# Kernel tuning notes

Hardware: AMD Instinct MI355X
Metric: run time of the kernel (lower is better)

Reference implementation:

```python
import jax, jax.numpy as jnp
import numpy as np

N, T_PLUS_1, D_IN, WV, HID, V = 64, 33, 1024, 512, 1024, 32000
NULL_IDX = 0


def setup_inputs() -> dict:
    key = jax.random.key(0)
    ks = jax.random.split(key, 9)
    return {
        "features": jax.random.normal(ks[0], (N, D_IN, 4, 4), jnp.float32),
        "captions": jax.random.randint(ks[1], (N, T_PLUS_1), 0, V),
        "W_embed": jax.random.normal(ks[2], (V, WV), jnp.float32) / np.float32(np.sqrt(V)),
        "Wx": jax.random.normal(ks[3], (WV, 4 * HID), jnp.float32) / np.float32(np.sqrt(WV)),
        "Wh": jax.random.normal(ks[4], (HID, 4 * HID), jnp.float32) / np.float32(np.sqrt(HID)),
        "Wattn": jax.random.normal(ks[5], (HID, 4 * HID), jnp.float32) / np.float32(np.sqrt(HID)),
        "b": jnp.zeros((4 * HID,), jnp.float32),
        "W_proj": jax.random.normal(ks[6], (D_IN, HID), jnp.float32) / np.float32(np.sqrt(D_IN)),
        "b_proj": jnp.zeros((HID,), jnp.float32),
        "W_out": jax.random.normal(ks[7], (HID, V), jnp.float32) / np.float32(np.sqrt(HID)),
        "b_out": jnp.zeros((V,), jnp.float32),
    }


def reference(features, captions, W_embed, Wx, Wh, Wattn, b, W_proj, b_proj, W_out, b_out):
    n, _ = captions.shape
    cap_in = captions[:, :-1]   # [N, T]
    cap_out = captions[:, 1:]   # [N, T]

    # project_input applied channel-last: A is [N, H, 4, 4]
    A = jnp.einsum('ndhw,dk->nkhw', features, W_proj) + b_proj[None, :, None, None]
    h0 = A.mean(axis=(2, 3))  # [N, H]
    c0 = h0
    hdim = h0.shape[1]
    A_flat = A.reshape(n, hdim, -1)  # [N, H, P] with P = 16 grid cells
    inv_sqrt_h = jnp.float32(1.0 / np.sqrt(hdim))

    x = W_embed[cap_in]  # [N, T, WV]

    def step(carry, x_t):
        prev_h, prev_c = carry
        # dot-product attention over the spatial grid
        s = jnp.einsum('nh,nhp->np', prev_h, A_flat) * inv_sqrt_h
        w = jax.nn.softmax(s, axis=-1)
        attn = jnp.einsum('nhp,np->nh', A_flat, w)
        # LSTM gating
        a = x_t @ Wx + prev_h @ Wh + attn @ Wattn + b
        i = jax.nn.sigmoid(a[:, :hdim])
        f = jax.nn.sigmoid(a[:, hdim:2 * hdim])
        o = jax.nn.sigmoid(a[:, 2 * hdim:3 * hdim])
        g = jnp.tanh(a[:, 3 * hdim:])
        next_c = f * prev_c + i * g
        next_h = o * jnp.tanh(next_c)
        return (next_h, next_c), next_h

    _, hs = jax.lax.scan(step, (h0, c0), x.transpose(1, 0, 2))  # hs: [T, N, H]
    h = hs.transpose(1, 0, 2)  # [N, T, H]

    scores = h @ W_out + b_out  # [N, T, V]
    logp = jax.nn.log_softmax(scores, axis=-1)
    nll = -jnp.take_along_axis(logp, cap_out[..., None], axis=-1)[..., 0]  # [N, T]
    mask = (cap_out != NULL_IDX).astype(nll.dtype)
    loss = jnp.sum(nll * mask) / n
    return loss
```

## Files before the change

### kernel.cpp

```cpp
#include <hip/hip_runtime.h>
#include <hip/hip_bf16.h>
#include <math.h>

typedef __attribute__((ext_vector_type(8))) short short8;
typedef __attribute__((ext_vector_type(4))) float f32x4;
typedef unsigned short ushort_t;
typedef unsigned int uint_t;

typedef __attribute__((address_space(1))) const void gvoid_t;
typedef __attribute__((address_space(3))) void lvoid_t;

#define VTILES 125

static __device__ __forceinline__ ushort_t f2b(float f){
  __hip_bfloat16 h = __float2bfloat16(f);
  return *reinterpret_cast<ushort_t*>(&h);
}
static __device__ __forceinline__ float b2f(ushort_t u){
  __hip_bfloat16 h = *reinterpret_cast<__hip_bfloat16*>(&u);
  return __bfloat162float(h);
}
static __device__ __forceinline__ float sigmoidf_(float x){ return 1.0f/(1.0f+__expf(-x)); }

__global__ void k_transpose_cvt(const float* __restrict__ src, ushort_t* __restrict__ dst,
                                int C, int dstride, int dcoloff) {
  __shared__ ushort_t tile[64][72];
  int cb = blockIdx.x * 64, rb = blockIdx.y * 64;
  int tid = threadIdx.x;
  for (int it = 0; it < 4; ++it) {
    int e = tid + it*256;
    int row = e >> 4;
    int seg = e & 15;
    float4 v = *reinterpret_cast<const float4*>(&src[(size_t)(rb+row)*C + cb + seg*4]);
    tile[seg*4+0][row] = f2b(v.x);
    tile[seg*4+1][row] = f2b(v.y);
    tile[seg*4+2][row] = f2b(v.z);
    tile[seg*4+3][row] = f2b(v.w);
  }
  __syncthreads();
  for (int it = 0; it < 2; ++it) {
    int e = tid + it*256;
    int cl = e >> 3;
    int seg = e & 7;
    uint4 v = *reinterpret_cast<uint4*>(&tile[cl][seg*8]);
    *reinterpret_cast<uint4*>(&dst[(size_t)(cb+cl)*dstride + dcoloff + rb + seg*8]) = v;
  }
}

__global__ void k_featT(const float* __restrict__ feat, ushort_t* __restrict__ fBT) {
  __shared__ ushort_t t[16][264];
  int n = blockIdx.x;
  int tid = threadIdx.x;
  for (int it = 0; it < 4; ++it) {
    int d = it*256 + tid;
    const float* src = &feat[((size_t)n*1024 + d)*16];
    #pragma unroll
    for (int q = 0; q < 4; ++q) {
      float4 v = *reinterpret_cast<const float4*>(&src[q*4]);
      t[q*4+0][tid] = f2b(v.x);
      t[q*4+1][tid] = f2b(v.y);
      t[q*4+2][tid] = f2b(v.z);
      t[q*4+3][tid] = f2b(v.w);
    }
    __syncthreads();
    #pragma unroll
    for (int w = 0; w < 2; ++w) {
      int e = tid + w*256;
      int p = e >> 5;
      int seg = e & 31;
      uint4 v = *reinterpret_cast<uint4*>(&t[p][seg*8]);
      *reinterpret_cast<uint4*>(&fBT[((size_t)n*16 + p)*1024 + it*256 + seg*8]) = v;
    }
    __syncthreads();
  }
}

__global__ void k_embed(const int* __restrict__ captions, const float* __restrict__ W_embed,
                        ushort_t* __restrict__ xb) {
  int e = (blockIdx.x*256 + threadIdx.x) * 4;
  int nt = e >> 9;
  int n = nt >> 5, t = nt & 31;
  int col = e & 511;
  int tok = captions[n*33 + t];
  float4 v = *reinterpret_cast<const float4*>(&W_embed[(size_t)tok*512 + col]);
  ushort4 o; o.x=f2b(v.x); o.y=f2b(v.y); o.z=f2b(v.z); o.w=f2b(v.w);
  *reinterpret_cast<ushort4*>(&xb[e]) = o;
}

__global__ void k_projmm(const ushort_t* __restrict__ WprojT, const ushort_t* __restrict__ fBT,
                         const float* __restrict__ b_proj, float* __restrict__ A_flat,
                         ushort_t* __restrict__ Abt, float* __restrict__ hbuf) {
  __shared__ ushort_t As[64*64];
  __shared__ ushort_t Bs[64*64];
  int kt = blockIdx.x, nt = blockIdx.y;
  int k0 = kt*64, n0 = nt*64;
  int tid = threadIdx.x;
  int wave = tid>>6, lane = tid&63, lr = lane&15, lg = lane>>4;
  int srow = lane>>3, sxor8 = ((lane&7)^srow)*8;
  f32x4 acc[4];
  #pragma unroll
  for (int nf=0;nf<4;++nf) acc[nf] = (f32x4){0.f,0.f,0.f,0.f};
  for (int kc = 0; kc < 1024; kc += 64){
    __syncthreads();
    #pragma unroll
    for (int u = 0; u < 2; ++u){
      int r0 = wave*16 + u*8;
      const ushort_t* srcA = &WprojT[(size_t)(k0 + r0 + srow)*1024 + kc + sxor8];
      const ushort_t* srcB = &fBT[(size_t)(n0 + r0 + srow)*1024 + kc + sxor8];
      __builtin_amdgcn_global_load_lds((gvoid_t*)srcA, (lvoid_t*)&As[r0*64], 16, 0, 0);
      __builtin_amdgcn_global_load_lds((gvoid_t*)srcB, (lvoid_t*)&Bs[r0*64], 16, 0, 0);
    }
    __syncthreads();
    #pragma unroll
    for (int kk = 0; kk < 2; ++kk){
      int swz = (((kk*4 + lg) ^ (lr & 7)) * 8);
      short8 af = *reinterpret_cast<short8*>(&As[(wave*16 + lr)*64 + swz]);
      #pragma unroll
      for (int nf = 0; nf < 4; ++nf){
        short8 bf = *reinterpret_cast<short8*>(&Bs[(nf*16 + lr)*64 + swz]);
        acc[nf] = __builtin_amdgcn_mfma_f32_16x16x32_bf16(af, bf, acc[nf], 0, 0, 0);
      }
    }
  }
  #pragma unroll
  for (int nf=0;nf<4;++nf){
    int ncol = n0 + nf*16 + lr;
    int nidx = ncol >> 4, p = ncol & 15;
    ushort4 ab;
    #pragma unroll
    for (int r=0;r<4;++r){
      int kh = k0 + wave*16 + lg*4 + r;
      float val = acc[nf][r] + b_proj[kh];
      A_flat[((size_t)nidx*1024 + kh)*16 + p] = val;
      (&ab.x)[r] = f2b(val);
      float s = val;
      s += __shfl_xor(s, 1, 64);
      s += __shfl_xor(s, 2, 64);
      s += __shfl_xor(s, 4, 64);
      s += __shfl_xor(s, 8, 64);
      if (lr == 0) hbuf[(nt*4 + nf)*1024 + kh] = s * (1.f/16.f);
    }
    *reinterpret_cast<ushort4*>(&Abt[(size_t)ncol*1024 + k0 + wave*16 + lg*4]) = ab;
  }
}

__global__ void k_pmm(const ushort_t* __restrict__ WcatT, const ushort_t* __restrict__ Abt,
                      ushort_t* __restrict__ P3) {
  __shared__ ushort_t As[64*64];
  __shared__ ushort_t Bs[64*64];
  __shared__ ushort_t Dt2[64][72];
  int jt = blockIdx.x, nt = blockIdx.y;
  int j0 = jt*64, n0 = nt*64;
  int tid = threadIdx.x;
  int wave = tid>>6, lane = tid&63, lr = lane&15, lg = lane>>4;
  int srow = lane>>3, sxor8 = ((lane&7)^srow)*8;
  f32x4 acc[4];
  #pragma unroll
  for (int nf=0;nf<4;++nf) acc[nf] = (f32x4){0.f,0.f,0.f,0.f};
  for (int kc = 0; kc < 1024; kc += 64){
    __syncthreads();
    #pragma unroll
    for (int u = 0; u < 2; ++u){
      int r0 = wave*16 + u*8;
      const ushort_t* srcA = &WcatT[(size_t)(j0 + r0 + srow)*2560 + 1536 + kc + sxor8];
      const ushort_t* srcB = &Abt[(size_t)(n0 + r0 + srow)*1024 + kc + sxor8];
      __builtin_amdgcn_global_load_lds((gvoid_t*)srcA, (lvoid_t*)&As[r0*64], 16, 0, 0);
      __builtin_amdgcn_global_load_lds((gvoid_t*)srcB, (lvoid_t*)&Bs[r0*64], 16, 0, 0);
    }
    __syncthreads();
    #pragma unroll
    for (int kk = 0; kk < 2; ++kk){
      int swz = (((kk*4 + lg) ^ (lr & 7)) * 8);
      short8 af = *reinterpret_cast<short8*>(&As[(wave*16 + lr)*64 + swz]);
      #pragma unroll
      for (int nf = 0; nf < 4; ++nf){
        short8 bf = *reinterpret_cast<short8*>(&Bs[(nf*16 + lr)*64 + swz]);
        acc[nf] = __builtin_amdgcn_mfma_f32_16x16x32_bf16(af, bf, acc[nf], 0, 0, 0);
      }
    }
  }
  __syncthreads();
  #pragma unroll
  for (int nf=0;nf<4;++nf)
    #pragma unroll
    for (int r=0;r<4;++r)
      Dt2[wave*16 + lg*4 + r][nf*16 + lr] = f2b(acc[nf][r]);
  __syncthreads();
  #pragma unroll
  for (int it=0; it<2; ++it){
    int e = it*256 + tid;
    int row = e >> 3, seg = e & 7;
    uint4 v = *reinterpret_cast<uint4*>(&Dt2[row][seg*8]);
    *reinterpret_cast<uint4*>(&P3[(((size_t)nt*4 + (seg>>1))*4096 + j0 + row)*16 + (seg&1)*8]) = v;
  }
}

__global__ void k_xmm(const ushort_t* __restrict__ WcatT, const ushort_t* __restrict__ xb,
                      ushort_t* __restrict__ xpre) {
  __shared__ ushort_t As[64*64];
  __shared__ ushort_t Bs[64*64];
  __shared__ float Dt[64][68];
  int jt = blockIdx.x, mt = blockIdx.y;
  int j0 = jt*64, m0 = mt*64;
  int tid = threadIdx.x;
  int wave = tid>>6, lane = tid&63, lr = lane&15, lg = lane>>4;
  int srow = lane>>3, sxor8 = ((lane&7)^srow)*8;
  f32x4 acc[4];
  #pragma unroll
  for (int nf=0;nf<4;++nf) acc[nf] = (f32x4){0.f,0.f,0.f,0.f};
  for (int kc = 0; kc < 512; kc += 64){
    __syncthreads();
    #pragma unroll
    for (int u = 0; u < 2; ++u){
      int r0 = wave*16 + u*8;
      const ushort_t* srcA = &WcatT[(size_t)(j0 + r0 + srow)*2560 + kc + sxor8];
      const ushort_t* srcB = &xb[(size_t)(m0 + r0 + srow)*512 + kc + sxor8];
      __builtin_amdgcn_global_load_lds((gvoid_t*)srcA, (lvoid_t*)&As[r0*64], 16, 0, 0);
      __builtin_amdgcn_global_load_lds((gvoid_t*)srcB, (lvoid_t*)&Bs[r0*64], 16, 0, 0);
    }
    __syncthreads();
    #pragma unroll
    for (int kk = 0; kk < 2; ++kk){
      int swz = (((kk*4 + lg) ^ (lr & 7)) * 8);
      short8 af = *reinterpret_cast<short8*>(&As[(wave*16 + lr)*64 + swz]);
      #pragma unroll
      for (int nf = 0; nf < 4; ++nf){
        short8 bf = *reinterpret_cast<short8*>(&Bs[(nf*16 + lr)*64 + swz]);
        acc[nf] = __builtin_amdgcn_mfma_f32_16x16x32_bf16(af, bf, acc[nf], 0, 0, 0);
      }
    }
  }
  __syncthreads();
  #pragma unroll
  for (int nf=0; nf<4; ++nf)
    #pragma unroll
    for (int r=0;r<4;++r)
      Dt[nf*16+lr][wave*16 + lg*4 + r] = acc[nf][r];
  __syncthreads();
  #pragma unroll
  for (int it=0; it<4; ++it){
    int e = tid + it*256;
    int nrow = e >> 4, seg = e & 15;
    float4 v = *reinterpret_cast<float4*>(&Dt[nrow][seg*4]);
    ushort4 o; o.x=f2b(v.x); o.y=f2b(v.y); o.z=f2b(v.z); o.w=f2b(v.w);
    *reinterpret_cast<ushort4*>(&xpre[(size_t)(m0+nrow)*4096 + j0 + seg*4]) = o;
  }
}

__global__ void k_gate(int i, const ushort_t* __restrict__ xpre, const float* __restrict__ a_part,
                       const float* __restrict__ bvec, const ushort_t* __restrict__ P3,
                       const float* __restrict__ A_flat, const float* __restrict__ hbuf,
                       float* __restrict__ cbuf, const float* __restrict__ sp_rd,
                       float* __restrict__ sp_wr, ushort_t* __restrict__ hbf,
                       ushort_t* __restrict__ hall) {
  __shared__ float wvLds[16];
  __shared__ float wred[4][16];
  int n = blockIdx.x >> 2, sp = blockIdx.x & 3;
  int tid = threadIdx.x;
  int wave = tid>>6, lane = tid&63;
  int k = sp*256 + tid;
  float hv;
  if (i == 0){
    hv = hbuf[n*1024 + k];
    cbuf[n*1024 + k] = hv;
    hbf[n*1024 + k] = f2b(hv);
  } else {
    if (tid < 16){
      float sv = (sp_rd[(n*4+0)*16+tid] + sp_rd[(n*4+1)*16+tid] +
                  sp_rd[(n*4+2)*16+tid] + sp_rd[(n*4+3)*16+tid]) * (1.f/32.f);
      float m = sv;
      #pragma unroll
      for (int d=1; d<16; d<<=1) m = fmaxf(m, __shfl_xor(m, d, 64));
      float e = __expf(sv - m);
      float s = e;
      #pragma unroll
      for (int d=1; d<16; d<<=1) s += __shfl_xor(s, d, 64);
      wvLds[tid] = e / s;
    }
    __syncthreads();
    float wv[16];
    #pragma unroll
    for (int p=0;p<16;++p) wv[p] = wvLds[p];
    float av[4];
    #pragma unroll
    for (int g=0;g<4;++g){
      int j = g*1024 + k;
      float x = bvec[j] + b2f(xpre[(size_t)(n*32 + (i-1))*4096 + j]);
      #pragma unroll
      for (int ks=0;ks<8;++ks) x += a_part[((size_t)ks*64 + n)*4096 + j];
      const ushort_t* pp = &P3[((size_t)n*4096 + j)*16];
      short8 p0 = *reinterpret_cast<const short8*>(pp);
      short8 p1 = *reinterpret_cast<const short8*>(pp+8);
      #pragma unroll
      for (int p=0;p<8;++p) x += wv[p]*b2f((ushort_t)p0[p]);
      #pragma unroll
      for (int p=0;p<8;++p) x += wv[8+p]*b2f((ushort_t)p1[p]);
      av[g]=x;
    }
    float ig=sigmoidf_(av[0]), fg=sigmoidf_(av[1]), og=sigmoidf_(av[2]), gg=tanhf(av[3]);
    float c = fg*cbuf[n*1024+k] + ig*gg;
    hv = og*tanhf(c);
    cbuf[n*1024+k] = c;
    hall[((size_t)n*32 + (i-1))*1024 + k] = f2b(hv);
    if (i < 32) hbf[n*1024+k] = f2b(hv);
  }
  if (i == 32) return;
  float sacc[16];
  const float* An = &A_flat[((size_t)n*1024 + k)*16];
  #pragma unroll
  for (int p=0;p<16;p+=4){
    float4 a4 = *reinterpret_cast<const float4*>(&An[p]);
    sacc[p] = hv*a4.x; sacc[p+1] = hv*a4.y; sacc[p+2] = hv*a4.z; sacc[p+3] = hv*a4.w;
  }
  #pragma unroll
  for (int d=1; d<64; d<<=1)
    #pragma unroll
    for (int p=0;p<16;++p) sacc[p] += __shfl_xor(sacc[p], d, 64);
  if (lane == 0)
    #pragma unroll
    for (int p=0;p<16;++p) wred[wave][p] = sacc[p];
  __syncthreads();
  if (tid < 16)
    sp_wr[(n*4+sp)*16 + tid] = wred[0][tid]+wred[1][tid]+wred[2][tid]+wred[3][tid];
}

__global__ void k_mm(const ushort_t* __restrict__ WcatT, const ushort_t* __restrict__ hbf,
                     float* __restrict__ a_part) {
  __shared__ ushort_t As[64*64];
  __shared__ ushort_t Bs[64*64];
  __shared__ float Dt[64][68];
  int jt = blockIdx.x, ks = blockIdx.y;
  int j0 = jt*64;
  int tid = threadIdx.x;
  int wave = tid>>6, lane = tid&63, lr = lane&15, lg = lane>>4;
  int srow = lane>>3, sxor8 = ((lane&7)^srow)*8;
  f32x4 acc[4];
  #pragma unroll
  for (int nf=0;nf<4;++nf) acc[nf] = (f32x4){0.f,0.f,0.f,0.f};
  for (int kc = 0; kc < 128; kc += 64){
    __syncthreads();
    #pragma unroll
    for (int u = 0; u < 2; ++u){
      int r0 = wave*16 + u*8;
      const ushort_t* srcA = &WcatT[(size_t)(j0 + r0 + srow)*2560 + 512 + ks*128 + kc + sxor8];
      const ushort_t* srcB = &hbf[(size_t)(r0 + srow)*1024 + ks*128 + kc + sxor8];
      __builtin_amdgcn_global_load_lds((gvoid_t*)srcA, (lvoid_t*)&As[r0*64], 16, 0, 0);
      __builtin_amdgcn_global_load_lds((gvoid_t*)srcB, (lvoid_t*)&Bs[r0*64], 16, 0, 0);
    }
    __syncthreads();
    #pragma unroll
    for (int kk = 0; kk < 2; ++kk){
      int swz = (((kk*4 + lg) ^ (lr & 7)) * 8);
      short8 af = *reinterpret_cast<short8*>(&As[(wave*16 + lr)*64 + swz]);
      #pragma unroll
      for (int nf = 0; nf < 4; ++nf){
        short8 bf = *reinterpret_cast<short8*>(&Bs[(nf*16 + lr)*64 + swz]);
        acc[nf] = __builtin_amdgcn_mfma_f32_16x16x32_bf16(af, bf, acc[nf], 0, 0, 0);
      }
    }
  }
  __syncthreads();
  #pragma unroll
  for (int nf=0; nf<4; ++nf)
    #pragma unroll
    for (int r=0;r<4;++r)
      Dt[nf*16+lr][wave*16 + lg*4 + r] = acc[nf][r];
  __syncthreads();
  #pragma unroll
  for (int it=0; it<4; ++it){
    int e = tid + it*256;
    int nrow = e >> 4, seg = e & 15;
    float4 v = *reinterpret_cast<float4*>(&Dt[nrow][seg*4]);
    *reinterpret_cast<float4*>(&a_part[((size_t)ks*64 + nrow)*4096 + j0 + seg*4]) = v;
  }
}

__global__ void __launch_bounds__(512, 2)
k_score(const ushort_t* __restrict__ WoutT, const ushort_t* __restrict__ hall,
        const float* __restrict__ b_out,
        float* __restrict__ pmax, float* __restrict__ psum) {
  __shared__ ushort_t A_lds[3][16384];
  __shared__ ushort_t B_lds[3][8192];
  __shared__ float bLds[256];
  __shared__ float pmLds[2][128];
  __shared__ float psLds[2][128];

  int bid = blockIdx.x;
  int wg = (bid & 7) * 250 + (bid >> 3);
  int vb = wg >> 4, rb = wg & 15;
  size_t v0 = (size_t)vb * 256, r0 = (size_t)rb * 128;
  int tid = threadIdx.x;
  int wid = tid >> 6, lane = tid & 63;
  int wr = wid >> 2, wc = wid & 3;
  int lr = lane & 15, lg = lane >> 4;
  int srow = lane >> 3, sxor8 = ((lane & 7) ^ srow) * 8;

  const ushort_t* Abase = WoutT + v0*1024 + (size_t)srow*1024 + sxor8;
  const ushort_t* Bbase = hall  + r0*1024 + (size_t)srow*1024 + sxor8;

  auto stA = [&](int set, int u, int t){
    __builtin_amdgcn_global_load_lds(
      (gvoid_t*)(Abase + (size_t)(u*64 + wid*8)*1024 + t*64),
      (lvoid_t*)&A_lds[set][(u*64 + wid*8)*64], 16, 0, 0);
  };
  auto stB = [&](int set, int u, int t){
    __builtin_amdgcn_global_load_lds(
      (gvoid_t*)(Bbase + (size_t)(u*64 + wid*8)*1024 + t*64),
      (lvoid_t*)&B_lds[set][(u*64 + wid*8)*64], 16, 0, 0);
  };

  f32x4 acc[8][2];
  #pragma unroll
  for (int fi=0; fi<8; ++fi)
    #pragma unroll
    for (int fj=0; fj<2; ++fj) acc[fi][fj] = (f32x4){0.f,0.f,0.f,0.f};

  short8 afr[4][2], bfr[2][2];
  auto ldA = [&](int set, int qv){
    #pragma unroll
    for (int f=0; f<4; ++f)
      #pragma unroll
      for (int kk=0; kk<2; ++kk){
        int row = wr*128 + (qv*4+f)*16 + lr;
        afr[f][kk] = *reinterpret_cast<short8*>(&A_lds[set][row*64 + (((kk*4+lg)^(lr&7))*8)]);
      }
  };
  auto ldB = [&](int set){
    #pragma unroll
    for (int fj=0; fj<2; ++fj)
      #pragma unroll
      for (int kk=0; kk<2; ++kk){
        int row = wc*32 + fj*16 + lr;
        bfr[fj][kk] = *reinterpret_cast<short8*>(&B_lds[set][row*64 + (((kk*4+lg)^(lr&7))*8)]);
      }
  };
  auto mfma16 = [&](int qv){
    __builtin_amdgcn_s_setprio(1);
    #pragma unroll
    for (int f=0; f<4; ++f)
      #pragma unroll
      for (int fj=0; fj<2; ++fj)
        #pragma unroll
        for (int kk=0; kk<2; ++kk)
          acc[qv*4+f][fj] = __builtin_amdgcn_mfma_f32_16x16x32_bf16(
              afr[f][kk], bfr[fj][kk], acc[qv*4+f][fj], 0, 0, 0);
    __builtin_amdgcn_s_setprio(0);
  };

  stA(0,0,0); stA(0,1,0); stA(0,2,0); stA(0,3,0); stB(0,0,0); stB(0,1,0);
  stA(1,0,1); stA(1,1,1); stA(1,2,1); stA(1,3,1); stB(1,0,1); stB(1,1,1);
  asm volatile("s_waitcnt vmcnt(6)" ::: "memory");
  __builtin_amdgcn_s_barrier();
  __builtin_amdgcn_sched_barrier(0);

  for (int g = 0; g < 16; ++g){
    int s = g % 3, sn = (g + 2) % 3;
    int tn = g + 2;
    bool st = tn < 16;
    ldA(s, 0); ldB(s);
    if (st){ stA(sn,0,tn); stA(sn,1,tn); stA(sn,2,tn); }
    __builtin_amdgcn_sched_barrier(0);
    __builtin_amdgcn_s_barrier();
    __builtin_amdgcn_sched_barrier(0);
    mfma16(0);
    __builtin_amdgcn_sched_barrier(0);
    __builtin_amdgcn_s_barrier();
    __builtin_amdgcn_sched_barrier(0);
    ldA(s, 1);
    if (st){ stA(sn,3,tn); stB(sn,0,tn); stB(sn,1,tn); }
    if (g == 14)      { asm volatile("s_waitcnt vmcnt(0)" ::: "memory"); }
    else if (g < 14)  { asm volatile("s_waitcnt vmcnt(6)" ::: "memory"); }
    __builtin_amdgcn_sched_barrier(0);
    __builtin_amdgcn_s_barrier();
    __builtin_amdgcn_sched_barrier(0);
    mfma16(1);
    __builtin_amdgcn_sched_barrier(0);
    __builtin_amdgcn_s_barrier();
    __builtin_amdgcn_sched_barrier(0);
  }

  if (tid < 256) bLds[tid] = b_out[v0 + tid];
  __syncthreads();
  float pm_[2], ps_[2];
  #pragma unroll
  for (int fj=0; fj<2; ++fj){
    float m = -1e30f;
    #pragma unroll
    for (int fi=0; fi<8; ++fi)
      #pragma unroll
      for (int rr=0; rr<4; ++rr){
        float x = acc[fi][fj][rr] + bLds[wr*128 + fi*16 + lg*4 + rr];
        m = fmaxf(m, x);
      }
    float ssum = 0.f;
    #pragma unroll
    for (int fi=0; fi<8; ++fi)
      #pragma unroll
      for (int rr=0; rr<4; ++rr){
        float x = acc[fi][fj][rr] + bLds[wr*128 + fi*16 + lg*4 + rr];
        ssum += __expf(x - m);
      }
    #pragma unroll
    for (int d=16; d<=32; d<<=1){
      float om = __shfl_xor(m, d, 64);
      float os = __shfl_xor(ssum, d, 64);
      float nm = fmaxf(m, om);
      ssum = ssum*__expf(m-nm) + os*__expf(om-nm);
      m = nm;
    }
    pm_[fj] = m; ps_[fj] = ssum;
  }
  if (lg == 0){
    #pragma unroll
    for (int fj=0; fj<2; ++fj){
      pmLds[wr][wc*32 + fj*16 + lr] = pm_[fj];
      psLds[wr][wc*32 + fj*16 + lr] = ps_[fj];
    }
  }
  __syncthreads();
  if (tid < 128){
    float m0 = pmLds[0][tid], m1 = pmLds[1][tid];
    float m = fmaxf(m0, m1);
    float sv = psLds[0][tid]*__expf(m0-m) + psLds[1][tid]*__expf(m1-m);
    pmax[(size_t)(r0 + tid)*VTILES + vb] = m;
    psum[(size_t)(r0 + tid)*VTILES + vb] = sv;
  }
}

__global__ void k_nll(const ushort_t* __restrict__ hall, const ushort_t* __restrict__ WoutT,
                      const float* __restrict__ b_out, const int* __restrict__ captions,
                      const float* __restrict__ pmax, const float* __restrict__ psum,
                      float* __restrict__ row_loss) {
  int tid = threadIdx.x;
  int wave = tid>>6, lane = tid&63;
  int r = blockIdx.x*4 + wave;
  int n = r>>5, t = r&31;
  int y = captions[n*33 + t + 1];
  const ushort_t* hrow = hall + (size_t)r*1024;
  const ushort_t* wrow = WoutT + (size_t)y*1024;
  float dot = 0.f;
  #pragma unroll
  for (int i=0;i<2;++i){
    int off = lane*8 + i*512;
    short8 hv = *reinterpret_cast<const short8*>(&hrow[off]);
    short8 wv = *reinterpret_cast<const short8*>(&wrow[off]);
    #pragma unroll
    for (int e2=0;e2<8;++e2) dot += b2f((ushort_t)hv[e2])*b2f((ushort_t)wv[e2]);
  }
  float m = -1e30f, s = 0.f;
  for (int j = lane; j < VTILES; j += 64){
    float mj = pmax[(size_t)r*VTILES + j];
    float sj = psum[(size_t)r*VTILES + j];
    float nm = fmaxf(m, mj);
    s = s*__expf(m-nm) + sj*__expf(mj-nm);
    m = nm;
  }
  #pragma unroll
  for (int d=32; d>=1; d>>=1){
    dot += __shfl_xor(dot, d, 64);
    float om = __shfl_xor(m, d, 64);
    float os = __shfl_xor(s, d, 64);
    float nm = fmaxf(m, om);
    s = s*__expf(m-nm) + os*__expf(om-nm);
    m = nm;
  }
  if (lane==0){
    float lse = m + __logf(s);
    row_loss[r] = (y != 0) ? (lse - (dot + b_out[y])) : 0.f;
  }
}

__global__ void k_final(const float* __restrict__ row_loss, float* __restrict__ out) {
  __shared__ float red[256];
  int tid = threadIdx.x;
  float s = 0.f;
  #pragma unroll
  for (int i=0;i<8;++i) s += row_loss[tid + i*256];
  red[tid] = s;
  __syncthreads();
  for (int off=128; off>=1; off>>=1){
    if (tid<off) red[tid] += red[tid+off];
    __syncthreads();
  }
  if (tid==0) out[0] = red[0] * (1.f/64.f);
}

extern "C" void kernel_launch(void* const* d_in, const int* in_sizes, int n_in,
                              void* d_out, int out_size, void* d_ws, size_t ws_size,
                              hipStream_t stream) {
  const float* features = (const float*)d_in[0];
  const int*   captions = (const int*)d_in[1];
  const float* W_embed  = (const float*)d_in[2];
  const float* Wx       = (const float*)d_in[3];
  const float* Wh       = (const float*)d_in[4];
  const float* Wattn    = (const float*)d_in[5];
  const float* b        = (const float*)d_in[6];
  const float* W_proj   = (const float*)d_in[7];
  const float* b_proj   = (const float*)d_in[8];
  const float* W_out    = (const float*)d_in[9];
  const float* b_out    = (const float*)d_in[10];
  float* out = (float*)d_out;

  char* wsp = (char*)d_ws;
  size_t off = 0;
  auto alloc = [&](size_t bytes)->char*{
    char* p = wsp + off; off += (bytes + 255) & ~(size_t)255; return p;
  };
  ushort_t* WcatT  = (ushort_t*)alloc((size_t)4096*2560*2);
  ushort_t* WoutT  = (ushort_t*)alloc((size_t)32000*1024*2);
  ushort_t* WprojT = (ushort_t*)alloc((size_t)1024*1024*2);
  ushort_t* fBT    = (ushort_t*)alloc((size_t)1024*1024*2);
  ushort_t* Abt    = (ushort_t*)alloc((size_t)1024*1024*2);
  float* A_flat    = (float*)alloc((size_t)64*1024*16*4);
  ushort_t* xb     = (ushort_t*)alloc((size_t)64*32*512*2);
  float* hbuf      = (float*)alloc((size_t)64*1024*4);
  ushort_t* P3     = (ushort_t*)alloc((size_t)64*4096*16*2);
  ushort_t* xpre   = (ushort_t*)alloc((size_t)2048*4096*2);
  float* a_part    = (float*)alloc((size_t)8*64*4096*4);
  ushort_t* hbf    = (ushort_t*)alloc((size_t)64*1024*2);
  float* cbuf      = (float*)alloc((size_t)64*1024*4);
  float* spbuf     = (float*)alloc((size_t)2*64*4*16*4);
  ushort_t* hall   = (ushort_t*)alloc((size_t)2048*1024*2);
  float* pmax      = (float*)alloc((size_t)2048*VTILES*4);
  float* psum      = (float*)alloc((size_t)2048*VTILES*4);
  float* row_loss  = (float*)alloc((size_t)2048*4);

  hipLaunchKernelGGL(k_transpose_cvt, dim3(64, 8),   dim3(256), 0, stream, Wx,     WcatT,  4096, 2560, 0);
  hipLaunchKernelGGL(k_transpose_cvt, dim3(64, 16),  dim3(256), 0, stream, Wh,     WcatT,  4096, 2560, 512);
  hipLaunchKernelGGL(k_transpose_cvt, dim3(64, 16),  dim3(256), 0, stream, Wattn,  WcatT,  4096, 2560, 1536);
  hipLaunchKernelGGL(k_transpose_cvt, dim3(500, 16), dim3(256), 0, stream, W_out,  WoutT,  32000, 1024, 0);
  hipLaunchKernelGGL(k_transpose_cvt, dim3(16, 16),  dim3(256), 0, stream, W_proj, WprojT, 1024, 1024, 0);
  hipLaunchKernelGGL(k_featT, dim3(64), dim3(256), 0, stream, features, fBT);
  hipLaunchKernelGGL(k_embed, dim3(1024), dim3(256), 0, stream, captions, W_embed, xb);
  hipLaunchKernelGGL(k_projmm, dim3(16, 16), dim3(256), 0, stream, WprojT, fBT, b_proj, A_flat, Abt, hbuf);
  hipLaunchKernelGGL(k_pmm, dim3(64, 16), dim3(256), 0, stream, WcatT, Abt, P3);
  hipLaunchKernelGGL(k_xmm, dim3(64, 32), dim3(256), 0, stream, WcatT, xb, xpre);

  for (int i = 0; i <= 32; ++i){
    const float* sp_rd = spbuf + ((i+1)&1)*4096;
    float*       sp_wr = spbuf + (i&1)*4096;
    hipLaunchKernelGGL(k_gate, dim3(256), dim3(256), 0, stream, i, xpre, a_part, b, P3,
                       A_flat, hbuf, cbuf, sp_rd, sp_wr, hbf, hall);
    if (i < 32)
      hipLaunchKernelGGL(k_mm, dim3(64, 8), dim3(256), 0, stream, WcatT, hbf, a_part);
  }

  hipLaunchKernelGGL(k_score, dim3(2000), dim3(512), 0, stream, WoutT, hall, b_out, pmax, psum);
  hipLaunchKernelGGL(k_nll, dim3(512), dim3(256), 0, stream, hall, WoutT, b_out, captions, pmax, psum, row_loss);
  hipLaunchKernelGGL(k_final, dim3(1), dim3(256), 0, stream, row_loss, out);
}
```

Baseline: 673.8 us.

## Replace triple-buffered k_score pipeline with single-buffer loop at higher occupancy

Removes the hand-scheduled three-stage LDS ring buffer, with its explicit waitcnt, sched_barrier and setprio, from the vocab score GEMM. In its place is a simple single-buffered loop that loads each 64-wide K chunk, syncs, and computes. LDS per block shrinks to about a third, and launch_bounds asks for 4 blocks per CU, so the design relies on occupancy rather than intra-block overlap to hide global-load latency. The risk is that loads are now fully exposed within each block and there are two barriers per K step.

```diff
diff --git a/kernel.cpp b/kernel.cpp
--- a/kernel.cpp
+++ b/kernel.cpp
@@ -375,12 +375,12 @@
   }
 }
 
-__global__ void __launch_bounds__(512, 2)
+__global__ void __launch_bounds__(512, 4)
 k_score(const ushort_t* __restrict__ WoutT, const ushort_t* __restrict__ hall,
         const float* __restrict__ b_out,
         float* __restrict__ pmax, float* __restrict__ psum) {
-  __shared__ ushort_t A_lds[3][16384];
-  __shared__ ushort_t B_lds[3][8192];
+  __shared__ ushort_t A_lds[256*64];
+  __shared__ ushort_t B_lds[128*64];
   __shared__ float bLds[256];
   __shared__ float pmLds[2][128];
   __shared__ float psLds[2][128];
@@ -395,91 +395,44 @@
   int lr = lane & 15, lg = lane >> 4;
   int srow = lane >> 3, sxor8 = ((lane & 7) ^ srow) * 8;
 
+  if (tid < 256) bLds[tid] = b_out[v0 + tid];
+
   const ushort_t* Abase = WoutT + v0*1024 + (size_t)srow*1024 + sxor8;
   const ushort_t* Bbase = hall  + r0*1024 + (size_t)srow*1024 + sxor8;
 
-  auto stA = [&](int set, int u, int t){
-    __builtin_amdgcn_global_load_lds(
-      (gvoid_t*)(Abase + (size_t)(u*64 + wid*8)*1024 + t*64),
-      (lvoid_t*)&A_lds[set][(u*64 + wid*8)*64], 16, 0, 0);
-  };
-  auto stB = [&](int set, int u, int t){
-    __builtin_amdgcn_global_load_lds(
-      (gvoid_t*)(Bbase + (size_t)(u*64 + wid*8)*1024 + t*64),
-      (lvoid_t*)&B_lds[set][(u*64 + wid*8)*64], 16, 0, 0);
-  };
-
   f32x4 acc[8][2];
   #pragma unroll
   for (int fi=0; fi<8; ++fi)
     #pragma unroll
     for (int fj=0; fj<2; ++fj) acc[fi][fj] = (f32x4){0.f,0.f,0.f,0.f};
 
-  short8 afr[4][2], bfr[2][2];
-  auto ldA = [&](int set, int qv){
-    #pragma unroll
-    for (int f=0; f<4; ++f)
-      #pragma unroll
-      for (int kk=0; kk<2; ++kk){
-        int row = wr*128 + (qv*4+f)*16 + lr;
-        afr[f][kk] = *reinterpret_cast<short8*>(&A_lds[set][row*64 + (((kk*4+lg)^(lr&7))*8)]);
+  for (int kc = 0; kc < 1024; kc += 64) {
+    __syncthreads();
+    #pragma unroll
+    for (int u = 0; u < 4; ++u)
+      __builtin_amdgcn_global_load_lds(
+        (gvoid_t*)(Abase + (size_t)(u*64 + wid*8)*1024 + kc),
+        (lvoid_t*)&A_lds[(u*64 + wid*8)*64], 16, 0, 0);
+    #pragma unroll
+    for (int u = 0; u < 2; ++u)
+      __builtin_amdgcn_global_load_lds(
+        (gvoid_t*)(Bbase + (size_t)(u*64 + wid*8)*1024 + kc),
+        (lvoid_t*)&B_lds[(u*64 + wid*8)*64], 16, 0, 0);
+    __syncthreads();
+    #pragma unroll
+    for (int kk = 0; kk < 2; ++kk) {
+      int swz = ((kk*4 + lg) ^ (lr & 7)) << 3;
+      short8 bf0 = *reinterpret_cast<short8*>(&B_lds[(wc*32 + lr)*64 + swz]);
+      short8 bf1 = *reinterpret_cast<short8*>(&B_lds[(wc*32 + 16 + lr)*64 + swz]);
+      #pragma unroll
+      for (int fi = 0; fi < 8; ++fi) {
+        short8 af = *reinterpret_cast<short8*>(&A_lds[(wr*128 + fi*16 + lr)*64 + swz]);
+        acc[fi][0] = __builtin_amdgcn_mfma_f32_16x16x32_bf16(af, bf0, acc[fi][0], 0,0,0);
+        acc[fi][1] = __builtin_amdgcn_mfma_f32_16x16x32_bf16(af, bf1, acc[fi][1], 0,0,0);
       }
-  };
-  auto ldB = [&](int set){
-    #pragma unroll
-    for (int fj=0; fj<2; ++fj)
-      #pragma unroll
-      for (int kk=0; kk<2; ++kk){
-        int row = wc*32 + fj*16 + lr;
-        bfr[fj][kk] = *reinterpret_cast<short8*>(&B_lds[set][row*64 + (((kk*4+lg)^(lr&7))*8)]);
-      }
-  };
-  auto mfma16 = [&](int qv){
-    __builtin_amdgcn_s_setprio(1);
-    #pragma unroll
-    for (int f=0; f<4; ++f)
-      #pragma unroll
-      for (int fj=0; fj<2; ++fj)
-        #pragma unroll
-        for (int kk=0; kk<2; ++kk)
-          acc[qv*4+f][fj] = __builtin_amdgcn_mfma_f32_16x16x32_bf16(
-              afr[f][kk], bfr[fj][kk], acc[qv*4+f][fj], 0, 0, 0);
-    __builtin_amdgcn_s_setprio(0);
-  };
-
-  stA(0,0,0); stA(0,1,0); stA(0,2,0); stA(0,3,0); stB(0,0,0); stB(0,1,0);
-  stA(1,0,1); stA(1,1,1); stA(1,2,1); stA(1,3,1); stB(1,0,1); stB(1,1,1);
-  asm volatile("s_waitcnt vmcnt(6)" ::: "memory");
-  __builtin_amdgcn_s_barrier();
-  __builtin_amdgcn_sched_barrier(0);
-
-  for (int g = 0; g < 16; ++g){
-    int s = g % 3, sn = (g + 2) % 3;
-    int tn = g + 2;
-    bool st = tn < 16;
-    ldA(s, 0); ldB(s);
-    if (st){ stA(sn,0,tn); stA(sn,1,tn); stA(sn,2,tn); }
-    __builtin_amdgcn_sched_barrier(0);
-    __builtin_amdgcn_s_barrier();
-    __builtin_amdgcn_sched_barrier(0);
-    mfma16(0);
-    __builtin_amdgcn_sched_barrier(0);
-    __builtin_amdgcn_s_barrier();
-    __builtin_amdgcn_sched_barrier(0);
-    ldA(s, 1);
-    if (st){ stA(sn,3,tn); stB(sn,0,tn); stB(sn,1,tn); }
-    if (g == 14)      { asm volatile("s_waitcnt vmcnt(0)" ::: "memory"); }
-    else if (g < 14)  { asm volatile("s_waitcnt vmcnt(6)" ::: "memory"); }
-    __builtin_amdgcn_sched_barrier(0);
-    __builtin_amdgcn_s_barrier();
-    __builtin_amdgcn_sched_barrier(0);
-    mfma16(1);
-    __builtin_amdgcn_sched_barrier(0);
-    __builtin_amdgcn_s_barrier();
-    __builtin_amdgcn_sched_barrier(0);
-  }
-
-  if (tid < 256) bLds[tid] = b_out[v0 + tid];
+    }
+  }
+
   __syncthreads();
   float pm_[2], ps_[2];
   #pragma unroll
```

Result: faster. 637.9 us (-5.3%).
